# Kernel optimization log

Measured on AMD Instinct MI355X. Metric: run time of the kernel, lower is better.

Reference implementation:

```python
import jax, jax.numpy as jnp
import numpy as np

B, TAPE, N, F = 128, 100000, 50000, 32

def setup_inputs() -> dict:
    key = jax.random.key(0)
    k1, k2, k3, k4 = jax.random.split(key, 4)
    tape = jax.random.normal(k1, (B, TAPE), dtype=jnp.float32)
    input_indices = jax.random.randint(k2, (N, F), 0, TAPE)
    # He init scaled by fan-in, padding slots (index==0) zeroed as in __init__
    weights = jax.random.normal(k3, (N, F), dtype=jnp.float32) * jnp.sqrt(2.0 / F)
    weights = jnp.where(input_indices == 0, 0.0, weights)
    bias = jnp.zeros((N,), dtype=jnp.float32)
    output_indices = jnp.arange(N)
    act_type = jax.random.randint(k4, (N,), 0, 2)
    return {"tape": tape, "weights": weights, "bias": bias,
            "input_indices": input_indices, "output_indices": output_indices,
            "act_type": act_type}

def reference(tape, weights, bias, input_indices, output_indices, act_type):
    # gather padded fan-in inputs: [B, N, F]
    gathered = tape[:, input_indices]
    # weighted sum over fan-in + bias: [B, N]
    x = jnp.einsum('bnf,nf->bn', gathered, weights) + bias
    # per-activation-type apply (two activation groups: relu / tanh)
    x = jnp.where(act_type == 0, jax.nn.relu(x), jnp.tanh(x))
    # scatter results back into tape
    return tape.at[:, output_indices].set(x)
```

## Files before the change

### kernel.cpp

```cpp
#include <hip/hip_runtime.h>
#include <cmath>

#define TAPE_SZ 100000
#define N_SZ    50000
#define F_SZ    32
#define B_SZ    128
#define NCHUNK  8
#define CB      16
#define NB      125

static __device__ __forceinline__ unsigned short f32_to_bf16(float f) {
    unsigned int u = __float_as_uint(f);
    u = (u + 0x7fffu + ((u >> 16) & 1u)) >> 16;
    return (unsigned short)u;
}

__global__ __launch_bounds__(256) void transpose_tape(const float* __restrict__ in,
                                                      unsigned short* __restrict__ outT,
                                                      float* __restrict__ out) {
    __shared__ float tile[32 * 133];
    const int x0  = blockIdx.x * 32;
    const int tid = threadIdx.x;

    {
        const int xq = tid & 7;
        const int b0 = tid >> 3;
        const bool tail = (x0 + xq * 4 >= N_SZ);
        #pragma unroll
        for (int it = 0; it < 4; ++it) {
            const int b = b0 + it * 32;
            const float4 v = *(const float4*)(in + (size_t)b * TAPE_SZ + x0 + xq * 4);
            tile[(xq * 4 + 0) * 133 + b] = v.x;
            tile[(xq * 4 + 1) * 133 + b] = v.y;
            tile[(xq * 4 + 2) * 133 + b] = v.z;
            tile[(xq * 4 + 3) * 133 + b] = v.w;
            if (tail) *(float4*)(out + (size_t)b * TAPE_SZ + x0 + xq * 4) = v;
        }
    }
    __syncthreads();

    {
        const int s  = tid & 63;
        const int w  = tid >> 6;
        const int h  = s & 1;
        const int xr = s >> 1;
        #pragma unroll
        for (int j = 0; j < 2; ++j) {
            const int c = w + 4 * j;
            const float* src = &tile[xr * 133 + c * CB + h * 8];
            union { unsigned short u[8]; uint4 q; } pk;
            #pragma unroll
            for (int k = 0; k < 8; ++k) pk.u[k] = f32_to_bf16(src[k]);
            *(uint4*)(outT + ((size_t)c * TAPE_SZ + x0 + xr) * CB + h * 8) = pk.q;
        }
    }
}

__global__ __launch_bounds__(256) void gather_mm(const unsigned short* __restrict__ tapeT,
                                                 const float* __restrict__ weights,
                                                 const float* __restrict__ bias,
                                                 const int*   __restrict__ in_idx,
                                                 const int*   __restrict__ out_idx,
                                                 const int*   __restrict__ act_type,
                                                 float* __restrict__ out) {
    __shared__ int   s_idx[NB][33];
    __shared__ float s_w[NB][33];
    __shared__ float s_bias[NB];
    __shared__ int   s_act[NB];
    __shared__ int   s_oidx[NB];

    const int tid  = threadIdx.x;
    const int c    = blockIdx.x & 7;
    const int n0   = (blockIdx.x >> 3) * NB;
    const int nmax = (N_SZ - n0 < NB) ? (N_SZ - n0) : NB;

    const uint4*  gi = (const uint4*)(in_idx)   + (size_t)n0 * 8;
    const float4* gw = (const float4*)(weights) + (size_t)n0 * 8;
    for (int i = tid; i < nmax * 8; i += 256) {
        const int n  = i >> 3;
        const int f0 = (i & 7) * 4;
        const uint4  vi = gi[i];
        const float4 vw = gw[i];
        s_idx[n][f0 + 0] = vi.x;
        s_idx[n][f0 + 1] = vi.y;
        s_idx[n][f0 + 2] = vi.z;
        s_idx[n][f0 + 3] = vi.w;
        s_w[n][f0 + 0] = vw.x;
        s_w[n][f0 + 1] = vw.y;
        s_w[n][f0 + 2] = vw.z;
        s_w[n][f0 + 3] = vw.w;
    }
    if (tid < nmax) {
        s_bias[tid] = bias[n0 + tid];
        s_act[tid]  = act_type[n0 + tid];
        s_oidx[tid] = out_idx[n0 + tid];
    }
    __syncthreads();

    const int oct = tid & 1;
    const int nl  = tid >> 1;
    if (nl < nmax) {
        const unsigned short* base = tapeT + (size_t)c * TAPE_SZ * CB + oct * 8;
        float a0 = 0.f, a1 = 0.f, a2 = 0.f, a3 = 0.f, a4 = 0.f, a5 = 0.f, a6 = 0.f, a7 = 0.f;
        #pragma unroll
        for (int fo = 0; fo < 32; fo += 8) {
            int   i8[8]; float w8[8];
            #pragma unroll
            for (int j = 0; j < 8; ++j) { i8[j] = s_idx[nl][fo + j]; w8[j] = s_w[nl][fo + j]; }
            uint4 q8[8];
            #pragma unroll
            for (int j = 0; j < 8; ++j)
                q8[j] = *(const uint4*)(base + (size_t)i8[j] * CB);
            #pragma unroll
            for (int j = 0; j < 8; ++j) {
                const float w = w8[j];
                a0 = fmaf(__uint_as_float(q8[j].x << 16),         w, a0);
                a1 = fmaf(__uint_as_float(q8[j].x & 0xffff0000u), w, a1);
                a2 = fmaf(__uint_as_float(q8[j].y << 16),         w, a2);
                a3 = fmaf(__uint_as_float(q8[j].y & 0xffff0000u), w, a3);
                a4 = fmaf(__uint_as_float(q8[j].z << 16),         w, a4);
                a5 = fmaf(__uint_as_float(q8[j].z & 0xffff0000u), w, a5);
                a6 = fmaf(__uint_as_float(q8[j].w << 16),         w, a6);
                a7 = fmaf(__uint_as_float(q8[j].w & 0xffff0000u), w, a7);
            }
        }
        const float bz = s_bias[nl];
        a0 += bz; a1 += bz; a2 += bz; a3 += bz; a4 += bz; a5 += bz; a6 += bz; a7 += bz;
        if (s_act[nl] == 0) {
            a0 = fmaxf(a0, 0.f); a1 = fmaxf(a1, 0.f); a2 = fmaxf(a2, 0.f); a3 = fmaxf(a3, 0.f);
            a4 = fmaxf(a4, 0.f); a5 = fmaxf(a5, 0.f); a6 = fmaxf(a6, 0.f); a7 = fmaxf(a7, 0.f);
        } else {
            a0 = tanhf(a0); a1 = tanhf(a1); a2 = tanhf(a2); a3 = tanhf(a3);
            a4 = tanhf(a4); a5 = tanhf(a5); a6 = tanhf(a6); a7 = tanhf(a7);
        }
        const int oc = s_oidx[nl];
        const int bb = c * CB + oct * 8;
        out[(size_t)(bb + 0) * TAPE_SZ + oc] = a0;
        out[(size_t)(bb + 1) * TAPE_SZ + oc] = a1;
        out[(size_t)(bb + 2) * TAPE_SZ + oc] = a2;
        out[(size_t)(bb + 3) * TAPE_SZ + oc] = a3;
        out[(size_t)(bb + 4) * TAPE_SZ + oc] = a4;
        out[(size_t)(bb + 5) * TAPE_SZ + oc] = a5;
        out[(size_t)(bb + 6) * TAPE_SZ + oc] = a6;
        out[(size_t)(bb + 7) * TAPE_SZ + oc] = a7;
    }
}

__global__ __launch_bounds__(128) void gather_fallback(const float* __restrict__ tape,
                                                       const float* __restrict__ weights,
                                                       const float* __restrict__ bias,
                                                       const int*   __restrict__ in_idx,
                                                       const int*   __restrict__ out_idx,
                                                       const int*   __restrict__ act_type,
                                                       float* __restrict__ out) {
    const int n = blockIdx.x;
    const int b = threadIdx.x;
    float acc = 0.f;
    for (int f = 0; f < F_SZ; ++f) {
        acc += tape[(size_t)b * TAPE_SZ + in_idx[(size_t)n * F_SZ + f]] *
               weights[(size_t)n * F_SZ + f];
    }
    acc += bias[n];
    acc = (act_type[n] == 0) ? fmaxf(acc, 0.f) : tanhf(acc);
    out[(size_t)b * TAPE_SZ + out_idx[n]] = acc;
}

__global__ __launch_bounds__(256) void copy_tail_fb(const float* __restrict__ tape,
                                                    float* __restrict__ out) {
    const int n4 = (TAPE_SZ - N_SZ) / 4;
    int i = blockIdx.x * blockDim.x + threadIdx.x;
    int b = blockIdx.y;
    if (i < n4) {
        const float4* src = (const float4*)(tape + (size_t)b * TAPE_SZ + N_SZ);
        float4*       dst = (float4*)(out  + (size_t)b * TAPE_SZ + N_SZ);
        dst[i] = src[i];
    }
}

extern "C" void kernel_launch(void* const* d_in, const int* in_sizes, int n_in,
                              void* d_out, int out_size, void* d_ws, size_t ws_size,
                              hipStream_t stream) {
    const float* tape    = (const float*)d_in[0];
    const float* weights = (const float*)d_in[1];
    const float* bias    = (const float*)d_in[2];
    const int*   in_idx  = (const int*)d_in[3];
    const int*   out_idx = (const int*)d_in[4];
    const int*   act     = (const int*)d_in[5];
    float*       out     = (float*)d_out;

    const size_t need = (size_t)NCHUNK * TAPE_SZ * CB * sizeof(unsigned short);
    if (ws_size >= need) {
        unsigned short* tapeT = (unsigned short*)d_ws;
        transpose_tape<<<dim3(TAPE_SZ / 32), dim3(256), 0, stream>>>(tape, tapeT, out);
        const int ntiles = (N_SZ + NB - 1) / NB;
        gather_mm<<<dim3(ntiles * NCHUNK), dim3(256), 0, stream>>>(
            tapeT, weights, bias, in_idx, out_idx, act, out);
    } else {
        copy_tail_fb<<<dim3(((TAPE_SZ - N_SZ) / 4 + 255) / 256, B_SZ), 256, 0, stream>>>(tape, out);
        gather_fallback<<<dim3(N_SZ), 128, 0, stream>>>(
            tape, weights, bias, in_idx, out_idx, act, out);
    }
}
```

Measured before the change: 187.0 us.

## Move tail copy into gather kernel and drop shared-memory staging of indices

```diff
diff --git a/kernel.cpp b/kernel.cpp
--- a/kernel.cpp
+++ b/kernel.cpp
@@ -7,7 +7,11 @@
 #define B_SZ    128
 #define NCHUNK  8
 #define CB      16
-#define NB      125
+#define NB      128
+#define NTILE   391
+#define NGBLK   (NTILE * NCHUNK)
+#define NTAIL   512
+#define TAIL_F4 1600000
 
 static __device__ __forceinline__ unsigned short f32_to_bf16(float f) {
     unsigned int u = __float_as_uint(f);
@@ -16,16 +20,13 @@
 }
 
 __global__ __launch_bounds__(256) void transpose_tape(const float* __restrict__ in,
-                                                      unsigned short* __restrict__ outT,
-                                                      float* __restrict__ out) {
+                                                      unsigned short* __restrict__ outT) {
     __shared__ float tile[32 * 133];
     const int x0  = blockIdx.x * 32;
     const int tid = threadIdx.x;
-
     {
         const int xq = tid & 7;
         const int b0 = tid >> 3;
-        const bool tail = (x0 + xq * 4 >= N_SZ);
         #pragma unroll
         for (int it = 0; it < 4; ++it) {
             const int b = b0 + it * 32;
@@ -34,11 +35,9 @@
             tile[(xq * 4 + 1) * 133 + b] = v.y;
             tile[(xq * 4 + 2) * 133 + b] = v.z;
             tile[(xq * 4 + 3) * 133 + b] = v.w;
-            if (tail) *(float4*)(out + (size_t)b * TAPE_SZ + x0 + xq * 4) = v;
         }
     }
     __syncthreads();
-
     {
         const int s  = tid & 63;
         const int w  = tid >> 6;
@@ -62,88 +61,83 @@
                                                  const int*   __restrict__ in_idx,
                                                  const int*   __restrict__ out_idx,
                                                  const int*   __restrict__ act_type,
+                                                 const float* __restrict__ tape,
                                                  float* __restrict__ out) {
-    __shared__ int   s_idx[NB][33];
-    __shared__ float s_w[NB][33];
-    __shared__ float s_bias[NB];
-    __shared__ int   s_act[NB];
-    __shared__ int   s_oidx[NB];
+    const int tid = threadIdx.x;
 
-    const int tid  = threadIdx.x;
-    const int c    = blockIdx.x & 7;
-    const int n0   = (blockIdx.x >> 3) * NB;
-    const int nmax = (N_SZ - n0 < NB) ? (N_SZ - n0) : NB;
+    if (blockIdx.x >= NGBLK) {
+        const float4* src = (const float4*)tape;
+        float4*       dst = (float4*)out;
+        const int stride = NTAIL * 256;
+        for (int i = (blockIdx.x - NGBLK) * 256 + tid; i < TAIL_F4; i += stride) {
+            const int b = i / 12500;
+            const int j = i - b * 12500;
+            const int off = b * (TAPE_SZ / 4) + (N_SZ / 4) + j;
+            dst[off] = src[off];
+        }
+        return;
+    }
 
-    const uint4*  gi = (const uint4*)(in_idx)   + (size_t)n0 * 8;
-    const float4* gw = (const float4*)(weights) + (size_t)n0 * 8;
-    for (int i = tid; i < nmax * 8; i += 256) {
-        const int n  = i >> 3;
-        const int f0 = (i & 7) * 4;
-        const uint4  vi = gi[i];
-        const float4 vw = gw[i];
-        s_idx[n][f0 + 0] = vi.x;
-        s_idx[n][f0 + 1] = vi.y;
-        s_idx[n][f0 + 2] = vi.z;
-        s_idx[n][f0 + 3] = vi.w;
-        s_w[n][f0 + 0] = vw.x;
-        s_w[n][f0 + 1] = vw.y;
-        s_w[n][f0 + 2] = vw.z;
-        s_w[n][f0 + 3] = vw.w;
-    }
-    if (tid < nmax) {
-        s_bias[tid] = bias[n0 + tid];
-        s_act[tid]  = act_type[n0 + tid];
-        s_oidx[tid] = out_idx[n0 + tid];
-    }
-    __syncthreads();
-
+    const int c   = blockIdx.x & 7;
+    const int n0  = (blockIdx.x >> 3) * NB;
     const int oct = tid & 1;
     const int nl  = tid >> 1;
-    if (nl < nmax) {
-        const unsigned short* base = tapeT + (size_t)c * TAPE_SZ * CB + oct * 8;
-        float a0 = 0.f, a1 = 0.f, a2 = 0.f, a3 = 0.f, a4 = 0.f, a5 = 0.f, a6 = 0.f, a7 = 0.f;
+    const int n   = n0 + nl;
+    if (n >= N_SZ) return;
+
+    const uint4*  gi = (const uint4*)(in_idx  + (size_t)n * 32);
+    const float4* gw = (const float4*)(weights + (size_t)n * 32);
+    const unsigned short* base = tapeT + (size_t)c * TAPE_SZ * CB + oct * 8;
+
+    float a0 = 0.f, a1 = 0.f, a2 = 0.f, a3 = 0.f, a4 = 0.f, a5 = 0.f, a6 = 0.f, a7 = 0.f;
+
+    #pragma unroll
+    for (int fo = 0; fo < 4; ++fo) {
+        const uint4  ia = gi[fo * 2], ib = gi[fo * 2 + 1];
+        const float4 wa = gw[fo * 2], wb = gw[fo * 2 + 1];
+        uint4 q8[8];
+        q8[0] = *(const uint4*)(base + (size_t)ia.x * CB);
+        q8[1] = *(const uint4*)(base + (size_t)ia.y * CB);
+        q8[2] = *(const uint4*)(base + (size_t)ia.z * CB);
+        q8[3] = *(const uint4*)(base + (size_t)ia.w * CB);
+        q8[4] = *(const uint4*)(base + (size_t)ib.x * CB);
+        q8[5] = *(const uint4*)(base + (size_t)ib.y * CB);
+        q8[6] = *(const uint4*)(base + (size_t)ib.z * CB);
+        q8[7] = *(const uint4*)(base + (size_t)ib.w * CB);
+        const float w8[8] = { wa.x, wa.y, wa.z, wa.w, wb.x, wb.y, wb.z, wb.w };
         #pragma unroll
-        for (int fo = 0; fo < 32; fo += 8) {
-            int   i8[8]; float w8[8];
-            #pragma unroll
-            for (int j = 0; j < 8; ++j) { i8[j] = s_idx[nl][fo + j]; w8[j] = s_w[nl][fo + j]; }
-            uint4 q8[8];
-            #pragma unroll
-            for (int j = 0; j < 8; ++j)
-                q8[j] = *(const uint4*)(base + (size_t)i8[j] * CB);
-            #pragma unroll
-            for (int j = 0; j < 8; ++j) {
-                const float w = w8[j];
-                a0 = fmaf(__uint_as_float(q8[j].x << 16),         w, a0);
-                a1 = fmaf(__uint_as_float(q8[j].x & 0xffff0000u), w, a1);
-                a2 = fmaf(__uint_as_float(q8[j].y << 16),         w, a2);
-                a3 = fmaf(__uint_as_float(q8[j].y & 0xffff0000u), w, a3);
-                a4 = fmaf(__uint_as_float(q8[j].z << 16),         w, a4);
-                a5 = fmaf(__uint_as_float(q8[j].z & 0xffff0000u), w, a5);
-                a6 = fmaf(__uint_as_float(q8[j].w << 16),         w, a6);
-                a7 = fmaf(__uint_as_float(q8[j].w & 0xffff0000u), w, a7);
-            }
+        for (int j = 0; j < 8; ++j) {
+            const float w = w8[j];
+            a0 = fmaf(__uint_as_float(q8[j].x << 16),         w, a0);
+            a1 = fmaf(__uint_as_float(q8[j].x & 0xffff0000u), w, a1);
+            a2 = fmaf(__uint_as_float(q8[j].y << 16),         w, a2);
+            a3 = fmaf(__uint_as_float(q8[j].y & 0xffff0000u), w, a3);
+            a4 = fmaf(__uint_as_float(q8[j].z << 16),         w, a4);
+            a5 = fmaf(__uint_as_float(q8[j].z & 0xffff0000u), w, a5);
+            a6 = fmaf(__uint_as_float(q8[j].w << 16),         w, a6);
+            a7 = fmaf(__uint_as_float(q8[j].w & 0xffff0000u), w, a7);
         }
-        const float bz = s_bias[nl];
-        a0 += bz; a1 += bz; a2 += bz; a3 += bz; a4 += bz; a5 += bz; a6 += bz; a7 += bz;
-        if (s_act[nl] == 0) {
-            a0 = fmaxf(a0, 0.f); a1 = fmaxf(a1, 0.f); a2 = fmaxf(a2, 0.f); a3 = fmaxf(a3, 0.f);
-            a4 = fmaxf(a4, 0.f); a5 = fmaxf(a5, 0.f); a6 = fmaxf(a6, 0.f); a7 = fmaxf(a7, 0.f);
-        } else {
-            a0 = tanhf(a0); a1 = tanhf(a1); a2 = tanhf(a2); a3 = tanhf(a3);
-            a4 = tanhf(a4); a5 = tanhf(a5); a6 = tanhf(a6); a7 = tanhf(a7);
-        }
-        const int oc = s_oidx[nl];
-        const int bb = c * CB + oct * 8;
-        out[(size_t)(bb + 0) * TAPE_SZ + oc] = a0;
-        out[(size_t)(bb + 1) * TAPE_SZ + oc] = a1;
-        out[(size_t)(bb + 2) * TAPE_SZ + oc] = a2;
-        out[(size_t)(bb + 3) * TAPE_SZ + oc] = a3;
-        out[(size_t)(bb + 4) * TAPE_SZ + oc] = a4;
-        out[(size_t)(bb + 5) * TAPE_SZ + oc] = a5;
-        out[(size_t)(bb + 6) * TAPE_SZ + oc] = a6;
-        out[(size_t)(bb + 7) * TAPE_SZ + oc] = a7;
     }
+
+    const float bz = bias[n];
+    a0 += bz; a1 += bz; a2 += bz; a3 += bz; a4 += bz; a5 += bz; a6 += bz; a7 += bz;
+    if (act_type[n] == 0) {
+        a0 = fmaxf(a0, 0.f); a1 = fmaxf(a1, 0.f); a2 = fmaxf(a2, 0.f); a3 = fmaxf(a3, 0.f);
+        a4 = fmaxf(a4, 0.f); a5 = fmaxf(a5, 0.f); a6 = fmaxf(a6, 0.f); a7 = fmaxf(a7, 0.f);
+    } else {
+        a0 = tanhf(a0); a1 = tanhf(a1); a2 = tanhf(a2); a3 = tanhf(a3);
+        a4 = tanhf(a4); a5 = tanhf(a5); a6 = tanhf(a6); a7 = tanhf(a7);
+    }
+    const int oc = out_idx[n];
+    const int bb = c * CB + oct * 8;
+    out[(size_t)(bb + 0) * TAPE_SZ + oc] = a0;
+    out[(size_t)(bb + 1) * TAPE_SZ + oc] = a1;
+    out[(size_t)(bb + 2) * TAPE_SZ + oc] = a2;
+    out[(size_t)(bb + 3) * TAPE_SZ + oc] = a3;
+    out[(size_t)(bb + 4) * TAPE_SZ + oc] = a4;
+    out[(size_t)(bb + 5) * TAPE_SZ + oc] = a5;
+    out[(size_t)(bb + 6) * TAPE_SZ + oc] = a6;
+    out[(size_t)(bb + 7) * TAPE_SZ + oc] = a7;
 }
 
 __global__ __launch_bounds__(128) void gather_fallback(const float* __restrict__ tape,
@@ -191,10 +185,9 @@
     const size_t need = (size_t)NCHUNK * TAPE_SZ * CB * sizeof(unsigned short);
     if (ws_size >= need) {
         unsigned short* tapeT = (unsigned short*)d_ws;
-        transpose_tape<<<dim3(TAPE_SZ / 32), dim3(256), 0, stream>>>(tape, tapeT, out);
-        const int ntiles = (N_SZ + NB - 1) / NB;
-        gather_mm<<<dim3(ntiles * NCHUNK), dim3(256), 0, stream>>>(
-            tapeT, weights, bias, in_idx, out_idx, act, out);
+        transpose_tape<<<dim3(TAPE_SZ / 32), dim3(256), 0, stream>>>(tape, tapeT);
+        gather_mm<<<dim3(NGBLK + NTAIL), dim3(256), 0, stream>>>(
+            tapeT, weights, bias, in_idx, out_idx, act, tape, out);
     } else {
         copy_tail_fb<<<dim3(((TAPE_SZ - N_SZ) / 4 + 255) / 256, B_SZ), 256, 0, stream>>>(tape, out);
         gather_fallback<<<dim3(N_SZ), 128, 0, stream>>>(
```

Measured after the change: 215.9 us. 1.15x slower.
